# Kernel tuning notes

Hardware: AMD Instinct MI355X
Metric: run time of the kernel (lower is better)

The kernel has to match this reference:

```python
import jax, jax.numpy as jnp
import numpy as np

SQRT2 = 1.4142135623730951

def _oyzx2spin():
    # 0yzx -> (uu, ud, du, dd) spin projection matrix, complex64
    M = np.array([[1, 0, 1, 0],
                  [0, -1j, 0, 1],
                  [0, 1j, 0, 1],
                  [1, 0, -1, 0]], dtype=np.complex64) / SQRT2
    return jnp.asarray(M)


def setup_inputs() -> dict:
    key = jax.random.key(0)
    B, C_real, nL, nR = 65536, 8, 13, 13  # C_real = 2 * C_complex (soc_complex_doubling), C_complex % 4 == 0
    HR_in = jax.random.normal(key, (B, C_real, nL, nR), dtype=jnp.float32)
    return {"HR_in": HR_in}


def reference(HR_in):
    # Faithful translation of E3Hamiltonian._spin_projection with
    # real storage + soc_complex_doubling=True.
    B, C_real, nL, nR = HR_in.shape
    half = C_real // 2  # complex channel count
    # pack complex-doubled real storage into complex channels
    HR_c = jax.lax.complex(HR_in[:, :half], HR_in[:, half:])  # [B, half, nL, nR] complex
    n_chunks = half // 4
    HR_view = HR_c.reshape(B, n_chunks, 4, nL, nR)  # 4 = (0, y, z, x) spin components
    M = _oyzx2spin()  # [4(spin), 4(0yzx)]
    # project 0yzx components onto (uu, ud, du, dd) spin basis
    HR_proj = jnp.einsum('nkslr,ps->nkplr', HR_view, M)
    HR_proj_flat = HR_proj.reshape(B, half, nL, nR)
    # unpack back to real storage: [real-half | imag-half] along channel dim
    return jnp.concatenate([HR_proj_flat.real, HR_proj_flat.imag], axis=1)
```

## Files before the change

### kernel.cpp

```cpp
#include <hip/hip_runtime.h>


#define PLANE 169
#define CSTRIDE 1352
#define QUADS 338
#define WAVES 4
#define BLOCKS 1792

__global__ __launch_bounds__(256) void spin_proj_kernel(
    const float4* __restrict__ in, float4* __restrict__ out,
    int n_items, int W) {
    __shared__ float lds[WAVES * CSTRIDE];
    const int wave = threadIdx.x >> 6;
    const int lane = threadIdx.x & 63;
    float* slab = lds + wave * CSTRIDE;
    float4* slab4 = (float4*)slab;

    const int v0 = lane,        v1 = lane + 64,  v2 = lane + 128;
    const int v3 = lane + 192,  v4 = lane + 256, v5 = lane + 320;
    const bool has5 = (v5 < QUADS);

    int it = blockIdx.x * WAVES + wave;
    if (it >= n_items) return;

    float4 p0, p1, p2, p3, p4, p5;
    {
        const float4* __restrict__ g = in + (size_t)it * QUADS;
        p0 = g[v0]; p1 = g[v1]; p2 = g[v2]; p3 = g[v3]; p4 = g[v4];
        if (has5) p5 = g[v5];
    }

    const float sc = 0.70710678118654752440f;

    while (it < n_items) {
        slab4[v0] = p0; slab4[v1] = p1; slab4[v2] = p2;
        slab4[v3] = p3; slab4[v4] = p4;
        if (has5) slab4[v5] = p5;

        const int nx = it + W;
        if (nx < n_items) {
            const float4* __restrict__ g = in + (size_t)nx * QUADS;
            p0 = g[v0]; p1 = g[v1]; p2 = g[v2]; p3 = g[v3]; p4 = g[v4];
            if (has5) p5 = g[v5];
        }

        asm volatile("s_waitcnt lgkmcnt(0)" ::: "memory");
        __builtin_amdgcn_wave_barrier();

        #pragma unroll
        for (int k = 0; k < 3; ++k) {
            const int j = lane + k * 64;
            if (k < 2 || j < PLANE) {
                float r0 = slab[0*PLANE + j], r1 = slab[1*PLANE + j];
                float r2 = slab[2*PLANE + j], r3 = slab[3*PLANE + j];
                float i0 = slab[4*PLANE + j], i1 = slab[5*PLANE + j];
                float i2 = slab[6*PLANE + j], i3 = slab[7*PLANE + j];
                slab[0*PLANE + j] = (r0 + r2) * sc;
                slab[1*PLANE + j] = (i1 + r3) * sc;
                slab[2*PLANE + j] = (r3 - i1) * sc;
                slab[3*PLANE + j] = (r0 - r2) * sc;
                slab[4*PLANE + j] = (i0 + i2) * sc;
                slab[5*PLANE + j] = (i3 - r1) * sc;
                slab[6*PLANE + j] = (r1 + i3) * sc;
                slab[7*PLANE + j] = (i0 - i2) * sc;
            }
        }

        asm volatile("s_waitcnt lgkmcnt(0)" ::: "memory");
        __builtin_amdgcn_wave_barrier();

        {
            float4* __restrict__ g = out + (size_t)it * QUADS;
            g[v0] = slab4[v0]; g[v1] = slab4[v1]; g[v2] = slab4[v2];
            g[v3] = slab4[v3]; g[v4] = slab4[v4];
            if (has5) g[v5] = slab4[v5];
        }

        it = nx;
    }
}

extern "C" void kernel_launch(void* const* d_in, const int* in_sizes, int n_in,
                              void* d_out, int out_size, void* d_ws, size_t ws_size,
                              hipStream_t stream) {
    const float4* in = (const float4*)d_in[0];
    float4* out = (float4*)d_out;

    const int n_items = in_sizes[0] / CSTRIDE;
    int grid = BLOCKS;
    int max_grid = (n_items + WAVES - 1) / WAVES;
    if (grid > max_grid) grid = max_grid;
    const int W = grid * WAVES;

    spin_proj_kernel<<<grid, 256, 0, stream>>>(in, out, n_items, W);
}
```

Before: 141.2 us.

## Stage input directly into double-buffered LDS with async global_load_lds

Replaces the register-staged prefetch (global load to VGPRs, then LDS write) with direct global-to-LDS async loads into a per-wave double buffer. The next item's loads are issued before computing the current one, and a `vmcnt(6)` wait replaces the LDS-count waits. Blocks shrink from 4 to 2 waves at the same grid size, which halves the resident waves in exchange for a deeper per-wave pipeline. The counter-based wait relies on exact instruction counts. It looks unsafe on the final iteration, where no new loads are issued, so the current buffer may not yet be fully loaded when it is read.

```diff
diff --git a/kernel.cpp b/kernel.cpp
--- a/kernel.cpp
+++ b/kernel.cpp
@@ -4,78 +4,83 @@
 #define PLANE 169
 #define CSTRIDE 1352
 #define QUADS 338
-#define WAVES 4
+#define TAIL 18
+#define WPB 2
 #define BLOCKS 1792
 
-__global__ __launch_bounds__(256) void spin_proj_kernel(
+typedef __attribute__((address_space(1))) const void g_as1;
+typedef __attribute__((address_space(3))) void l_as3;
+
+__device__ __forceinline__ void gload16(const void* gp, void* lp) {
+    g_as1* g = (g_as1*)(uintptr_t)gp;
+    l_as3* l = (l_as3*)(uint32_t)(uintptr_t)lp;
+    __builtin_amdgcn_global_load_lds(g, l, 16, 0, 0);
+}
+
+__device__ __forceinline__ void stage_item(const float4* __restrict__ g,
+                                           float4* slab4, int lane) {
+    #pragma unroll
+    for (int k = 0; k < 5; ++k)
+        gload16(g + k * 64 + lane, slab4 + k * 64);
+    if (lane < TAIL)
+        gload16(g + 320 + lane, slab4 + 320);
+}
+
+__global__ __launch_bounds__(128) void spin_proj_kernel(
     const float4* __restrict__ in, float4* __restrict__ out,
     int n_items, int W) {
-    __shared__ float lds[WAVES * CSTRIDE];
+    __shared__ float lds[WPB * 2 * CSTRIDE];
     const int wave = threadIdx.x >> 6;
     const int lane = threadIdx.x & 63;
-    float* slab = lds + wave * CSTRIDE;
-    float4* slab4 = (float4*)slab;
 
-    const int v0 = lane,        v1 = lane + 64,  v2 = lane + 128;
-    const int v3 = lane + 192,  v4 = lane + 256, v5 = lane + 320;
-    const bool has5 = (v5 < QUADS);
+    float* cur = lds + wave * 2 * CSTRIDE;
+    float* nxt = cur + CSTRIDE;
 
-    int it = blockIdx.x * WAVES + wave;
+    int it = blockIdx.x * WPB + wave;
     if (it >= n_items) return;
 
-    float4 p0, p1, p2, p3, p4, p5;
-    {
-        const float4* __restrict__ g = in + (size_t)it * QUADS;
-        p0 = g[v0]; p1 = g[v1]; p2 = g[v2]; p3 = g[v3]; p4 = g[v4];
-        if (has5) p5 = g[v5];
-    }
+    stage_item(in + (size_t)it * QUADS, (float4*)cur, lane);
 
     const float sc = 0.70710678118654752440f;
 
     while (it < n_items) {
-        slab4[v0] = p0; slab4[v1] = p1; slab4[v2] = p2;
-        slab4[v3] = p3; slab4[v4] = p4;
-        if (has5) slab4[v5] = p5;
+        const int nx = it + W;
+        if (nx < n_items)
+            stage_item(in + (size_t)nx * QUADS, (float4*)nxt, lane);
 
-        const int nx = it + W;
-        if (nx < n_items) {
-            const float4* __restrict__ g = in + (size_t)nx * QUADS;
-            p0 = g[v0]; p1 = g[v1]; p2 = g[v2]; p3 = g[v3]; p4 = g[v4];
-            if (has5) p5 = g[v5];
-        }
-
-        asm volatile("s_waitcnt lgkmcnt(0)" ::: "memory");
-        __builtin_amdgcn_wave_barrier();
+        asm volatile("s_waitcnt vmcnt(6)" ::: "memory");
+        __builtin_amdgcn_sched_barrier(0);
 
         #pragma unroll
         for (int k = 0; k < 3; ++k) {
             const int j = lane + k * 64;
             if (k < 2 || j < PLANE) {
-                float r0 = slab[0*PLANE + j], r1 = slab[1*PLANE + j];
-                float r2 = slab[2*PLANE + j], r3 = slab[3*PLANE + j];
-                float i0 = slab[4*PLANE + j], i1 = slab[5*PLANE + j];
-                float i2 = slab[6*PLANE + j], i3 = slab[7*PLANE + j];
-                slab[0*PLANE + j] = (r0 + r2) * sc;
-                slab[1*PLANE + j] = (i1 + r3) * sc;
-                slab[2*PLANE + j] = (r3 - i1) * sc;
-                slab[3*PLANE + j] = (r0 - r2) * sc;
-                slab[4*PLANE + j] = (i0 + i2) * sc;
-                slab[5*PLANE + j] = (i3 - r1) * sc;
-                slab[6*PLANE + j] = (r1 + i3) * sc;
-                slab[7*PLANE + j] = (i0 - i2) * sc;
+                float r0 = cur[0*PLANE + j], r1 = cur[1*PLANE + j];
+                float r2 = cur[2*PLANE + j], r3 = cur[3*PLANE + j];
+                float i0 = cur[4*PLANE + j], i1 = cur[5*PLANE + j];
+                float i2 = cur[6*PLANE + j], i3 = cur[7*PLANE + j];
+                cur[0*PLANE + j] = (r0 + r2) * sc;
+                cur[1*PLANE + j] = (i1 + r3) * sc;
+                cur[2*PLANE + j] = (r3 - i1) * sc;
+                cur[3*PLANE + j] = (r0 - r2) * sc;
+                cur[4*PLANE + j] = (i0 + i2) * sc;
+                cur[5*PLANE + j] = (i3 - r1) * sc;
+                cur[6*PLANE + j] = (r1 + i3) * sc;
+                cur[7*PLANE + j] = (i0 - i2) * sc;
             }
         }
 
-        asm volatile("s_waitcnt lgkmcnt(0)" ::: "memory");
-        __builtin_amdgcn_wave_barrier();
-
         {
             float4* __restrict__ g = out + (size_t)it * QUADS;
-            g[v0] = slab4[v0]; g[v1] = slab4[v1]; g[v2] = slab4[v2];
-            g[v3] = slab4[v3]; g[v4] = slab4[v4];
-            if (has5) g[v5] = slab4[v5];
+            const float4* slab4 = (const float4*)cur;
+            #pragma unroll
+            for (int k = 0; k < 5; ++k)
+                g[lane + k * 64] = slab4[lane + k * 64];
+            if (lane < TAIL)
+                g[320 + lane] = slab4[320 + lane];
         }
 
+        float* tmp = cur; cur = nxt; nxt = tmp;
         it = nx;
     }
 }
@@ -88,9 +93,9 @@
 
     const int n_items = in_sizes[0] / CSTRIDE;
     int grid = BLOCKS;
-    int max_grid = (n_items + WAVES - 1) / WAVES;
+    int max_grid = (n_items + WPB - 1) / WPB;
     if (grid > max_grid) grid = max_grid;
-    const int W = grid * WAVES;
+    const int W = grid * WPB;
 
-    spin_proj_kernel<<<grid, 256, 0, stream>>>(in, out, n_items, W);
+    spin_proj_kernel<<<grid, 128, 0, stream>>>(in, out, n_items, W);
 }
```

After: 149.9 us. 1.06x slower.
